# Kernel tuning notes

Hardware: AMD Instinct MI355X
Metric: run time of the kernel (lower is better)

## Reference

```python
import jax, jax.numpy as jnp
import numpy as np
from jax import lax

KH = KW = 3
K = KH * KW
STRIDE = 1
PAD = 1
DIL = 1
GN_GROUPS = 32
EPS = 1e-5


def setup_inputs() -> dict:
    key = jax.random.key(0)
    k0, k1, k2 = jax.random.split(key, 3)
    B, C, H, W = 8, 256, 64, 64
    O = 256
    x = jax.random.normal(k0, (B, C, H, W), jnp.float32)
    # offset-predicting conv (DeformConv2dPack.conv_offset); small weights keep offsets ~O(1)
    w_off = jax.random.normal(k1, (2 * K, C, KH, KW), jnp.float32) * 0.01
    b_off = jnp.zeros((2 * K,), jnp.float32)
    w_dcn = jax.random.normal(k2, (O, C, KH, KW), jnp.float32) * (1.0 / np.sqrt(C * K))
    gamma = jnp.ones((O,), jnp.float32)
    beta = jnp.zeros((O,), jnp.float32)
    return {"x": x, "w_off": w_off, "b_off": b_off, "w_dcn": w_dcn, "gamma": gamma, "beta": beta}


def _deform_conv(x, w_off, b_off, w_dcn):
    B, C, H, W = x.shape
    O = w_dcn.shape[0]
    # offsets via standard conv: [B, 2K, Ho, Wo]; channel layout (k, (dy, dx))
    offset = lax.conv_general_dilated(
        x, w_off, (STRIDE, STRIDE), [(PAD, PAD), (PAD, PAD)],
        rhs_dilation=(DIL, DIL), dimension_numbers=("NCHW", "OIHW", "NCHW"))
    offset = offset + b_off[None, :, None, None]
    Ho, Wo = offset.shape[2], offset.shape[3]
    off = offset.reshape(B, K, 2, Ho, Wo)
    ky = jnp.repeat(jnp.arange(KH), KW)  # [K]
    kx = jnp.tile(jnp.arange(KW), KH)    # [K]
    base_y = (jnp.arange(Ho) * STRIDE - PAD)[None, :, None] + (ky * DIL)[:, None, None]  # [K,Ho,1]
    base_x = (jnp.arange(Wo) * STRIDE - PAD)[None, None, :] + (kx * DIL)[:, None, None]  # [K,1,Wo]
    py = off[:, :, 0] + base_y[None].astype(off.dtype)  # [B,K,Ho,Wo]
    px = off[:, :, 1] + base_x[None].astype(off.dtype)

    def sample_one(xi, py_i, px_i):  # xi [C,H,W]; py/px [K,Ho,Wo]
        y0 = jnp.floor(py_i)
        x0 = jnp.floor(px_i)
        dy = py_i - y0
        dx = px_i - x0
        y0i = y0.astype(jnp.int32)
        x0i = x0.astype(jnp.int32)

        def gather(yi, xj, w):
            valid = (yi >= 0) & (yi < H) & (xj >= 0) & (xj < W)
            yc = jnp.clip(yi, 0, H - 1)
            xc = jnp.clip(xj, 0, W - 1)
            return xi[:, yc, xc] * (w * valid)[None]  # [C,K,Ho,Wo]

        return (gather(y0i, x0i, (1 - dy) * (1 - dx))
                + gather(y0i, x0i + 1, (1 - dy) * dx)
                + gather(y0i + 1, x0i, dy * (1 - dx))
                + gather(y0i + 1, x0i + 1, dy * dx))

    cols = jax.vmap(sample_one)(x, py, px)  # [B,C,K,Ho,Wo]
    y = jnp.einsum("ock,bckp->bop", w_dcn.reshape(O, C, K),
                   cols.reshape(B, C, K, Ho * Wo))
    return y.reshape(B, O, Ho, Wo)


def _group_norm(y, gamma, beta):
    B, O, Ho, Wo = y.shape
    g = y.reshape(B, GN_GROUPS, O // GN_GROUPS, Ho, Wo)
    mean = g.mean(axis=(2, 3, 4), keepdims=True)
    var = g.var(axis=(2, 3, 4), keepdims=True)
    yn = ((g - mean) * lax.rsqrt(var + EPS)).reshape(B, O, Ho, Wo)
    return yn * gamma[None, :, None, None] + beta[None, :, None, None]


def reference(x, w_off, b_off, w_dcn, gamma, beta):
    y = _deform_conv(x, w_off, b_off, w_dcn)
    y = _group_norm(y, gamma, beta)
    return y * jnp.tanh(jax.nn.softplus(y))  # Mish
```

## Files before the change

### kernel.cpp

```cpp
#include <hip/hip_runtime.h>
#include <hip/hip_bf16.h>
#include <math.h>

typedef __bf16 bf16x8 __attribute__((ext_vector_type(8)));
typedef float f32x4 __attribute__((ext_vector_type(4)));
typedef float f32x2 __attribute__((ext_vector_type(2)));
typedef unsigned int u32;
typedef u32 u32x4 __attribute__((ext_vector_type(4)));
typedef u32 u32x2 __attribute__((ext_vector_type(2)));


#define FENCE() __builtin_amdgcn_sched_barrier(0)
#define VMCNT(n) do { asm volatile("s_waitcnt vmcnt(" #n ")" ::: "memory"); FENCE(); } while (0)
#define LGKM0() do { asm volatile("s_waitcnt lgkmcnt(0)" ::: "memory"); FENCE(); } while (0)

__device__ inline u32 pack2bf16(float a, float b) {
  u32 ua = __float_as_uint(a);
  u32 ub = __float_as_uint(b);
  ua += 0x7fffu + ((ua >> 16) & 1u);
  ub += 0x7fffu + ((ub >> 16) & 1u);
  return (ua >> 16) | (ub & 0xffff0000u);
}

__global__ void prep(const float* __restrict__ w_dcn, const float* __restrict__ w_off,
                     unsigned short* __restrict__ wT4, unsigned short* __restrict__ wOffT,
                     float* __restrict__ stats) {
  size_t id = (size_t)blockIdx.x * 256 + threadIdx.x;
  if (id < 589824) {
    int o  = (int)(id / 2304);
    int ck = (int)(id % 2304);
    int k = ck >> 8, c = ck & 255;
    float v = w_dcn[(size_t)(o * 256 + c) * 9 + k];
    u32 uv = __float_as_uint(v);
    uv += 0x7fffu + ((uv >> 16) & 1u);
    int tile = ck >> 6, kk = ck & 63;
    int lin = o * 128 + kk * 2;
    int swz = lin ^ ((o & 7) << 4);
    *(unsigned short*)((char*)wT4 + (size_t)tile * 32768 + swz) = (unsigned short)(uv >> 16);
  } else if (id < 663552) {
    int r = (int)(id - 589824);
    int tile = r >> 11;
    int rr = r & 2047;
    int o = rr >> 6, kk = rr & 63;
    int k = tile >> 2, cc = tile & 3;
    int c = (cc << 6) + kk;
    float v = (o < 18) ? w_off[(size_t)(o * 256 + c) * 9 + k] : 0.f;
    u32 uv = __float_as_uint(v);
    uv += 0x7fffu + ((uv >> 16) & 1u);
    int swz = (o * 128 + kk * 2) ^ ((o & 7) << 4);
    *(unsigned short*)((char*)wOffT + (size_t)tile * 4096 + swz) = (unsigned short)(uv >> 16);
  } else if (id < 664064) {
    stats[id - 663552] = 0.f;
  }
}

__global__ __launch_bounds__(256) void transpose_x(const float* __restrict__ x,
                                                   unsigned short* __restrict__ xT) {
  __shared__ float tl[64][65];
  int bx = blockIdx.x;
  int b = bx >> 8;
  int y = (bx >> 2) & 63;
  int cb = (bx & 3) << 6;
  int t = threadIdx.x;
  int xi = t & 63, cr = t >> 6;
  size_t base = (((size_t)(b * 256 + cb) * 64 + y) << 6);
#pragma unroll
  for (int rep = 0; rep < 16; ++rep) {
    int cl = rep * 4 + cr;
    tl[cl][xi] = x[base + (size_t)cl * 4096 + xi];
  }
  __syncthreads();
  int xw = t & 63, cpair = t >> 6;
#pragma unroll
  for (int r = 0; r < 2; ++r) {
    int cgl = cpair * 2 + r;
    int cg = (cb >> 3) + cgl;
    u32 pk4[4];
#pragma unroll
    for (int i = 0; i < 4; ++i)
      pk4[i] = pack2bf16(tl[cgl * 8 + 2 * i][xw], tl[cgl * 8 + 2 * i + 1][xw]);
    u32x4 v = {pk4[0], pk4[1], pk4[2], pk4[3]};
    *(u32x4*)((char*)xT + (((size_t)b << 21)) + ((size_t)cg << 16) + ((y << 6) + xw) * 16) = v;
  }
}

__global__ __launch_bounds__(256) void conv_offset_mfma(
    const unsigned short* __restrict__ xT, const unsigned short* __restrict__ wOffT,
    float* __restrict__ offs) {
  __shared__ union {
    unsigned short Bo[4][2][2048];
    float red[4][64][32];
  } sm;
  const int bx = blockIdx.x;
  const int lb = ((bx & 7) << 6) + (bx >> 3);
  const int b = lb >> 6;
  const int row = lb & 63;
  const int t = threadIdx.x;
  const int lane = t & 63, w = t >> 6;
  const char* xTbB = (const char*)xT + ((size_t)b << 21);

  f32x4 acc[4][2];
#pragma unroll
  for (int i = 0; i < 4; ++i)
#pragma unroll
    for (int j = 0; j < 2; ++j) {
      f32x4 z = {0.f, 0.f, 0.f, 0.f};
      acc[i][j] = z;
    }

  auto stageB = [&](int k, int d) {
    const char* src = (const char*)wOffT + ((size_t)((k << 2) + w) << 12);
    char* dstb = (char*)&sm.Bo[w][d][0];
#pragma unroll
    for (int i2 = 0; i2 < 4; ++i2) {
      __builtin_amdgcn_global_load_lds(
          (const __attribute__((address_space(1))) u32*)(src + (i2 << 10) + (lane << 4)),
          (__attribute__((address_space(3))) u32*)(dstb + (i2 << 10)),
          16, 0, 0);
    }
  };

  stageB(0, 0);
  u32x4 rA[8];
  const u32x4 zv = {0u, 0u, 0u, 0u};

  for (int k = 0; k < 9; ++k) {
    int ky = k / 3, kxv = k - ky * 3;
    int rowp = row - 1 + ky;
    bool rok = ((unsigned)rowp < 64u);
    bool ok[4];
    if (rok) {
      int pix[4];
#pragma unroll
      for (int pg = 0; pg < 4; ++pg) {
        int xs = (pg << 4) + (lane & 15) + kxv - 1;
        ok[pg] = ((unsigned)xs < 64u);
        int xc = min(max(xs, 0), 63);
        pix[pg] = (rowp << 6) + xc;
      }
#pragma unroll
      for (int s = 0; s < 2; ++s) {
        const char* base = xTbB + ((size_t)((w << 3) + (s << 2) + (lane >> 4)) << 16);
#pragma unroll
        for (int pg = 0; pg < 4; ++pg)
          rA[s * 4 + pg] = *(const u32x4*)(base + ((size_t)pix[pg] << 4));
      }
    }
    if (k < 8) stageB(k + 1, (k + 1) & 1);
    VMCNT(4);
    if (rok) {
      const char* Bb = (const char*)&sm.Bo[w][k & 1][0];
#pragma unroll
      for (int s = 0; s < 2; ++s) {
        bf16x8 bb[2];
        int kx = (s << 6) + ((lane >> 4) << 4);
#pragma unroll
        for (int j = 0; j < 2; ++j) {
          int o = (j << 4) + (lane & 15);
          bb[j] = *(const bf16x8*)(Bb + o * 128 + (kx ^ ((o & 7) << 4)));
        }
#pragma unroll
        for (int pg = 0; pg < 4; ++pg) {
          u32x4 av = ok[pg] ? rA[s * 4 + pg] : zv;
          bf16x8 af = __builtin_bit_cast(bf16x8, av);
#pragma unroll
          for (int j = 0; j < 2; ++j)
            acc[pg][j] = __builtin_amdgcn_mfma_f32_16x16x32_bf16(af, bb[j], acc[pg][j], 0, 0, 0);
        }
      }
    }
  }

#pragma unroll
  for (int pg = 0; pg < 4; ++pg)
#pragma unroll
    for (int j = 0; j < 2; ++j)
#pragma unroll
      for (int r = 0; r < 4; ++r) {
        int px = (pg << 4) + ((lane >> 4) << 2) + r;
        int o = (j << 4) + (lane & 15);
        sm.red[w][px][o] = acc[pg][j][r];
      }
  __syncthreads();
  {
    int px = t >> 2, oq = (t & 3) << 3;
#pragma unroll
    for (int e = 0; e < 8; ++e) {
      int o = oq + e;
      if (o < 18) {
        float sv = sm.red[0][px][o] + sm.red[1][px][o]
                 + sm.red[2][px][o] + sm.red[3][px][o];
        offs[((size_t)b * 4096 + (row << 6) + px) * 18 + o] = sv;
      }
    }
  }
}

union ArenaM {
  struct {
    unsigned short A[2][128][64];
    unsigned short Bt[3][16384];
  } m;
  unsigned short ytile[256][136];
};

__global__ __launch_bounds__(512) void dcn_main(
    const unsigned short* __restrict__ xT, const float* __restrict__ offs,
    const float* __restrict__ boff, const unsigned short* __restrict__ wT4,
    unsigned short* __restrict__ yb, float* __restrict__ stats) {
  __shared__ ArenaM ar;
  __shared__ u32 pcor[9][128][2];
  __shared__ float pwt[9][128][4];

  const int bx = blockIdx.x;
  const int lb = ((bx & 7) << 5) + (bx >> 3);
  const int b = lb >> 5;
  const int pxbase = (lb & 31) << 7;
  const int t = threadIdx.x;
  const int lane = t & 63, wid = t >> 6;
  const char* xTbB = (const char*)xT + ((size_t)b << 21);
  const int pxs = ((wid & 1) << 6) + lane;
  const int gp = (wid >> 1) << 1;
  const int wr = wid >> 2, wc = wid & 3;
  const int obase = wc << 6;

  for (int idx = t; idx < 1152; idx += 512) {
    int k = idx >> 7, px = idx & 127;
    int pxg = pxbase + px;
    int yy = pxg >> 6, xx = pxg & 63;
    int ky = k / 3, kx = k - ky * 3;
    const float* op = offs + ((size_t)b * 4096 + pxg) * 18 + k * 2;
    float py = op[0] + boff[k * 2] + (float)(yy - 1 + ky);
    float pxf = op[1] + boff[k * 2 + 1] + (float)(xx - 1 + kx);
    float fy = floorf(py), fx = floorf(pxf);
    float dy = py - fy, dx = pxf - fx;
    int y0 = (int)fy, x0 = (int)fx;
    int y1 = y0 + 1, x1 = x0 + 1;
    float vy0 = ((unsigned)y0 < 64u) ? 1.f : 0.f;
    float vy1 = ((unsigned)y1 < 64u) ? 1.f : 0.f;
    float vx0 = ((unsigned)x0 < 64u) ? 1.f : 0.f;
    float vx1 = ((unsigned)x1 < 64u) ? 1.f : 0.f;
    int y0c = min(max(y0, 0), 63), y1c = min(max(y1, 0), 63);
    int x0c = min(max(x0, 0), 63), x1c = min(max(x1, 0), 63);
    pcor[k][px][0] = (u32)((y0c << 6) + x0c) | ((u32)((y0c << 6) + x1c) << 16);
    pcor[k][px][1] = (u32)((y1c << 6) + x0c) | ((u32)((y1c << 6) + x1c) << 16);
    pwt[k][px][0] = (1.f - dy) * (1.f - dx) * vy0 * vx0;
    pwt[k][px][1] = (1.f - dy) * dx * vy0 * vx1;
    pwt[k][px][2] = dy * (1.f - dx) * vy1 * vx0;
    pwt[k][px][3] = dy * dx * vy1 * vx1;
  }

  f32x4 acc[4][4];
#pragma unroll
  for (int i = 0; i < 4; ++i)
#pragma unroll
    for (int j = 0; j < 4; ++j) {
      f32x4 z = {0.f, 0.f, 0.f, 0.f};
      acc[i][j] = z;
    }

  __syncthreads();

  u32x4 rA[8];

  auto issueA = [&](int tt) {
    int k = tt >> 2, cc = tt & 3;
    u32 c01 = pcor[k][pxs][0], c23 = pcor[k][pxs][1];
    const char* p0 = xTbB + ((size_t)((cc << 3) + gp) << 16);
#pragma unroll
    for (int g = 0; g < 2; ++g) {
      const char* bgp = p0 + ((size_t)g << 16);
      rA[g * 4 + 0] = *(const u32x4*)(bgp + ((size_t)(c01 & 0xffffu) << 4));
      rA[g * 4 + 1] = *(const u32x4*)(bgp + ((size_t)(c01 >> 16) << 4));
      rA[g * 4 + 2] = *(const u32x4*)(bgp + ((size_t)(c23 & 0xffffu) << 4));
      rA[g * 4 + 3] = *(const u32x4*)(bgp + ((size_t)(c23 >> 16) << 4));
    }
  };
  auto issueB = [&](int tt, int bufi) {
    const char* src = (const char*)wT4 + ((size_t)tt << 15) + (wid << 12);
    char* dstb = (char*)&ar.m.Bt[bufi][0] + (wid << 12);
#pragma unroll
    for (int i2 = 0; i2 < 4; ++i2) {
      __builtin_amdgcn_global_load_lds(
          (const __attribute__((address_space(1))) u32*)(src + (i2 << 10) + (lane << 4)),
          (__attribute__((address_space(3))) u32*)(dstb + (i2 << 10)),
          16, 0, 0);
    }
  };
  auto blendA = [&](int tt) {
    int k = tt >> 2;
    f32x4 w = *(const f32x4*)&pwt[k][pxs][0];
    char* dst = (char*)&ar.m.A[tt & 1][0][0] + pxs * 128;
    int sw = (pxs & 7) << 4;
#pragma unroll
    for (int g = 0; g < 2; ++g) {
      u32 o4[4];
#pragma unroll
      for (int e = 0; e < 4; ++e) {
        u32 u0 = rA[g * 4 + 0][e], u1 = rA[g * 4 + 1][e];
        u32 u2 = rA[g * 4 + 2][e], u3 = rA[g * 4 + 3][e];
        float lo = w[0] * __uint_as_float(u0 << 16);
        lo = fmaf(w[1], __uint_as_float(u1 << 16), lo);
        lo = fmaf(w[2], __uint_as_float(u2 << 16), lo);
        lo = fmaf(w[3], __uint_as_float(u3 << 16), lo);
        float hi = w[0] * __uint_as_float(u0 & 0xffff0000u);
        hi = fmaf(w[1], __uint_as_float(u1 & 0xffff0000u), hi);
        hi = fmaf(w[2], __uint_as_float(u2 & 0xffff0000u), hi);
        hi = fmaf(w[3], __uint_as_float(u3 & 0xffff0000u), hi);
        asm("v_cvt_pk_bf16_f32 %0, %1, %2" : "=v"(o4[e]) : "v"(lo), "v"(hi));
      }
      u32x4 ov = {o4[0], o4[1], o4[2], o4[3]};
      *(u32x4*)(dst + (((gp + g) << 4) ^ sw)) = ov;
    }
  };

  issueA(0); FENCE();
  issueB(0, 0); FENCE();
  VMCNT(4);
  blendA(0);
  FENCE();
  issueA(1); FENCE();
  issueB(1, 1); FENCE();
  VMCNT(12);
  LGKM0();
  __builtin_amdgcn_s_barrier();

  int bm3 = 0;
  for (int tt = 0; tt < 36; ++tt) {
    {
      const char* Ab = (const char*)&ar.m.A[tt & 1][0][0];
      const char* Bb = (const char*)&ar.m.Bt[bm3][0];
      __builtin_amdgcn_s_setprio(1);
#pragma unroll
      for (int s = 0; s < 2; ++s) {
        int kx = (s << 6) + ((lane >> 4) << 4);
        bf16x8 a[4], bb[4];
#pragma unroll
        for (int i = 0; i < 4; ++i) {
          int r16 = (wr << 6) + (i << 4) + (lane & 15);
          a[i] = *(const bf16x8*)(Ab + r16 * 128 + (kx ^ ((r16 & 7) << 4)));
        }
#pragma unroll
        for (int j = 0; j < 4; ++j) {
          int o = obase + (j << 4) + (lane & 15);
          bb[j] = *(const bf16x8*)(Bb + o * 128 + (kx ^ ((o & 7) << 4)));
        }
#pragma unroll
        for (int i = 0; i < 4; ++i)
#pragma unroll
          for (int j = 0; j < 4; ++j)
            acc[i][j] = __builtin_amdgcn_mfma_f32_16x16x32_bf16(a[i], bb[j], acc[i][j], 0, 0, 0);
      }
      __builtin_amdgcn_s_setprio(0);
    }
    FENCE();
    if (tt < 35) {
      VMCNT(4);
      blendA(tt + 1);
      FENCE();
      if (tt < 34) {
        issueA(tt + 2); FENCE();
        int bn = bm3 + 2; if (bn >= 3) bn -= 3;
        issueB(tt + 2, bn); FENCE();
      }
    }
    if (tt == 34) { VMCNT(0); }
    else { VMCNT(12); }
    LGKM0();
    __builtin_amdgcn_s_barrier();
    FENCE();
    bm3 = (bm3 == 2) ? 0 : bm3 + 1;
  }

#pragma unroll
  for (int j = 0; j < 4; ++j) {
    float s1 = 0.f, s2 = 0.f;
#pragma unroll
    for (int i = 0; i < 4; ++i)
#pragma unroll
      for (int r = 0; r < 4; ++r) {
        float v = acc[i][j][r];
        s1 += v;
        s2 += v * v;
      }
    s1 += __shfl_xor(s1, 1, 64);  s2 += __shfl_xor(s2, 1, 64);
    s1 += __shfl_xor(s1, 2, 64);  s2 += __shfl_xor(s2, 2, 64);
    s1 += __shfl_xor(s1, 4, 64);  s2 += __shfl_xor(s2, 4, 64);
    s1 += __shfl_xor(s1, 16, 64); s2 += __shfl_xor(s2, 16, 64);
    s1 += __shfl_xor(s1, 32, 64); s2 += __shfl_xor(s2, 32, 64);
    if ((lane & 0x37) == 0) {
      int g = (obase + (j << 4) + (lane & 15)) >> 3;
      atomicAdd(&stats[((b << 5) + g) * 2 + 0], s1);
      atomicAdd(&stats[((b << 5) + g) * 2 + 1], s2);
    }
  }

#pragma unroll
  for (int i = 0; i < 4; ++i)
#pragma unroll
    for (int j = 0; j < 4; ++j) {
      int o = obase + (j << 4) + (lane & 15);
      int pxr = (wr << 6) + (i << 4) + ((lane >> 4) << 2);
      u32 wv0, wv1;
      asm("v_cvt_pk_bf16_f32 %0, %1, %2" : "=v"(wv0) : "v"(acc[i][j][0]), "v"(acc[i][j][1]));
      asm("v_cvt_pk_bf16_f32 %0, %1, %2" : "=v"(wv1) : "v"(acc[i][j][2]), "v"(acc[i][j][3]));
      u32x2 wv = {wv0, wv1};
      *(u32x2*)((char*)ar.ytile + o * 272 + pxr * 2) = wv;
    }
  __syncthreads();
  {
    int o = t >> 1, half = t & 1;
    const char* srcb = (const char*)ar.ytile + o * 272 + (half << 7);
    unsigned short* dst = yb + (((size_t)(b * 256 + o)) << 12) + pxbase + (half << 6);
#pragma unroll
    for (int qq = 0; qq < 8; ++qq)
      *(u32x4*)((char*)dst + (qq << 4)) = *(const u32x4*)(srcb + (qq << 4));
  }
}

__global__ __launch_bounds__(256) void gn_mish(const unsigned short* __restrict__ yb,
                                               const float* __restrict__ stats,
                                               const float* __restrict__ gamma,
                                               const float* __restrict__ beta,
                                               float* __restrict__ out) {
  int v = blockIdx.x * 512 + threadIdx.x;
#pragma unroll
  for (int it = 0; it < 2; ++it, v += 256) {
    int o = (v >> 9) & 255;
    int b = v >> 17;
    float s1 = stats[((b << 5) + (o >> 3)) * 2 + 0];
    float s2 = stats[((b << 5) + (o >> 3)) * 2 + 1];
    float mean = s1 * (1.f / 32768.f);
    float var = s2 * (1.f / 32768.f) - mean * mean;
    float rstd = rsqrtf(var + 1e-5f);
    float ga = gamma[o] * rstd, be = beta[o] - mean * gamma[o] * rstd;
    u32x4 u = *(const u32x4*)(yb + ((size_t)v << 3));
    float res[8];
#pragma unroll
    for (int e = 0; e < 4; ++e) {
      float va = __uint_as_float(u[e] << 16);
      float vb = __uint_as_float(u[e] & 0xffff0000u);
      float v0 = fmaf(va, ga, be);
      float v1 = fmaf(vb, ga, be);
      float e0 = expf(fminf(v0, 15.f));
      float e1 = expf(fminf(v1, 15.f));
      float n0 = e0 * (e0 + 2.f);
      float n1 = e1 * (e1 + 2.f);
      float m0 = v0 * (n0 / (n0 + 2.f));
      float m1 = v1 * (n1 / (n1 + 2.f));
      if (v0 > 15.f) m0 = v0;
      if (v1 > 15.f) m1 = v1;
      res[2 * e] = m0;
      res[2 * e + 1] = m1;
    }
    f32x4 o0 = {res[0], res[1], res[2], res[3]};
    f32x4 o1 = {res[4], res[5], res[6], res[7]};
    float* dst = out + ((size_t)v << 3);
    *(f32x4*)dst = o0;
    *((f32x4*)dst + 1) = o1;
  }
}

extern "C" void kernel_launch(void* const* d_in, const int* in_sizes, int n_in,
                              void* d_out, int out_size, void* d_ws, size_t ws_size,
                              hipStream_t stream) {
  const float* x     = (const float*)d_in[0];
  const float* w_off = (const float*)d_in[1];
  const float* b_off = (const float*)d_in[2];
  const float* w_dcn = (const float*)d_in[3];
  const float* gamma = (const float*)d_in[4];
  const float* beta  = (const float*)d_in[5];
  float* out = (float*)d_out;
  char* ws = (char*)d_ws;
  unsigned short* xT   = (unsigned short*)(ws);
  unsigned short* yb   = (unsigned short*)(ws + 16777216);
  float* offs          = (float*)(ws + 33554432);
  unsigned short* wT4  = (unsigned short*)(ws + 35913728);
  unsigned short* wOffT= (unsigned short*)(ws + 37093376);
  float* stats         = (float*)(ws + 37240832);
  prep<<<dim3(2594), dim3(256), 0, stream>>>(w_dcn, w_off, wT4, wOffT, stats);
  transpose_x<<<dim3(2048), dim3(256), 0, stream>>>(x, xT);
  conv_offset_mfma<<<dim3(512), dim3(256), 0, stream>>>(xT, wOffT, offs);
  dcn_main<<<dim3(256), dim3(512), 0, stream>>>(xT, offs, b_off, wT4, yb, stats);
  gn_mish<<<dim3(2048), dim3(256), 0, stream>>>(yb, stats, gamma, beta, out);
}
```

Before: 115.2 us.

## Shrink dcn_main tile to one 64-pixel row per 256-thread block

```diff
diff --git a/kernel.cpp b/kernel.cpp
--- a/kernel.cpp
+++ b/kernel.cpp
@@ -198,40 +198,49 @@
 
 union ArenaM {
   struct {
-    unsigned short A[2][128][64];
-    unsigned short Bt[3][16384];
+    unsigned short A[2][64][64];
+    unsigned short Bt[2][16384];
   } m;
-  unsigned short ytile[256][136];
+  unsigned short ytile[256][72];
 };
 
-__global__ __launch_bounds__(512) void dcn_main(
+__global__ __launch_bounds__(256) void dcn_main(
     const unsigned short* __restrict__ xT, const float* __restrict__ offs,
     const float* __restrict__ boff, const unsigned short* __restrict__ wT4,
     unsigned short* __restrict__ yb, float* __restrict__ stats) {
   __shared__ ArenaM ar;
-  __shared__ u32 pcor[9][128][2];
-  __shared__ float pwt[9][128][4];
+  __shared__ float sboff[18];
 
   const int bx = blockIdx.x;
-  const int lb = ((bx & 7) << 5) + (bx >> 3);
-  const int b = lb >> 5;
-  const int pxbase = (lb & 31) << 7;
+  const int lb = ((bx & 7) << 6) + (bx >> 3);
+  const int b = lb >> 6;
+  const int row = lb & 63;
+  const int pxbase = row << 6;
   const int t = threadIdx.x;
   const int lane = t & 63, wid = t >> 6;
   const char* xTbB = (const char*)xT + ((size_t)b << 21);
-  const int pxs = ((wid & 1) << 6) + lane;
-  const int gp = (wid >> 1) << 1;
-  const int wr = wid >> 2, wc = wid & 3;
-  const int obase = wc << 6;
-
-  for (int idx = t; idx < 1152; idx += 512) {
-    int k = idx >> 7, px = idx & 127;
-    int pxg = pxbase + px;
-    int yy = pxg >> 6, xx = pxg & 63;
+  const int gp = wid << 1;
+  const int obase = wid << 6;
+
+  if (t < 18) sboff[t] = boff[t];
+
+  f32x4 acc[4][4];
+#pragma unroll
+  for (int i = 0; i < 4; ++i)
+#pragma unroll
+    for (int j = 0; j < 4; ++j) {
+      f32x4 z = {0.f, 0.f, 0.f, 0.f};
+      acc[i][j] = z;
+    }
+
+  __syncthreads();
+
+  auto cparams = [&](int k, u32& c01, u32& c23, f32x4& w4) {
     int ky = k / 3, kx = k - ky * 3;
-    const float* op = offs + ((size_t)b * 4096 + pxg) * 18 + k * 2;
-    float py = op[0] + boff[k * 2] + (float)(yy - 1 + ky);
-    float pxf = op[1] + boff[k * 2 + 1] + (float)(xx - 1 + kx);
+    const float* op = offs + ((size_t)b * 4096 + pxbase + lane) * 18 + k * 2;
+    f32x2 o2 = *(const f32x2*)op;
+    float py = o2[0] + sboff[k * 2] + (float)(row - 1 + ky);
+    float pxf = o2[1] + sboff[k * 2 + 1] + (float)(lane - 1 + kx);
     float fy = floorf(py), fx = floorf(pxf);
     float dy = py - fy, dx = pxf - fx;
     int y0 = (int)fy, x0 = (int)fx;
@@ -242,31 +251,18 @@
     float vx1 = ((unsigned)x1 < 64u) ? 1.f : 0.f;
     int y0c = min(max(y0, 0), 63), y1c = min(max(y1, 0), 63);
     int x0c = min(max(x0, 0), 63), x1c = min(max(x1, 0), 63);
-    pcor[k][px][0] = (u32)((y0c << 6) + x0c) | ((u32)((y0c << 6) + x1c) << 16);
-    pcor[k][px][1] = (u32)((y1c << 6) + x0c) | ((u32)((y1c << 6) + x1c) << 16);
-    pwt[k][px][0] = (1.f - dy) * (1.f - dx) * vy0 * vx0;
-    pwt[k][px][1] = (1.f - dy) * dx * vy0 * vx1;
-    pwt[k][px][2] = dy * (1.f - dx) * vy1 * vx0;
-    pwt[k][px][3] = dy * dx * vy1 * vx1;
-  }
-
-  f32x4 acc[4][4];
-#pragma unroll
-  for (int i = 0; i < 4; ++i)
-#pragma unroll
-    for (int j = 0; j < 4; ++j) {
-      f32x4 z = {0.f, 0.f, 0.f, 0.f};
-      acc[i][j] = z;
-    }
-
-  __syncthreads();
+    c01 = (u32)((y0c << 6) + x0c) | ((u32)((y0c << 6) + x1c) << 16);
+    c23 = (u32)((y1c << 6) + x0c) | ((u32)((y1c << 6) + x1c) << 16);
+    w4[0] = (1.f - dy) * (1.f - dx) * vy0 * vx0;
+    w4[1] = (1.f - dy) * dx * vy0 * vx1;
+    w4[2] = dy * (1.f - dx) * vy1 * vx0;
+    w4[3] = dy * dx * vy1 * vx1;
+  };
 
   u32x4 rA[8];
 
-  auto issueA = [&](int tt) {
-    int k = tt >> 2, cc = tt & 3;
-    u32 c01 = pcor[k][pxs][0], c23 = pcor[k][pxs][1];
-    const char* p0 = xTbB + ((size_t)((cc << 3) + gp) << 16);
+  auto issueA = [&](int ccq, u32 c01, u32 c23) {
+    const char* p0 = xTbB + ((size_t)((ccq << 3) + gp) << 16);
 #pragma unroll
     for (int g = 0; g < 2; ++g) {
       const char* bgp = p0 + ((size_t)g << 16);
@@ -276,22 +272,20 @@
       rA[g * 4 + 3] = *(const u32x4*)(bgp + ((size_t)(c23 >> 16) << 4));
     }
   };
-  auto issueB = [&](int tt, int bufi) {
-    const char* src = (const char*)wT4 + ((size_t)tt << 15) + (wid << 12);
-    char* dstb = (char*)&ar.m.Bt[bufi][0] + (wid << 12);
-#pragma unroll
-    for (int i2 = 0; i2 < 4; ++i2) {
+  auto issueB = [&](int tt, int d) {
+    const char* src = (const char*)wT4 + ((size_t)tt << 15) + (wid << 13);
+    char* dstb = (char*)&ar.m.Bt[d][0] + (wid << 13);
+#pragma unroll
+    for (int i2 = 0; i2 < 8; ++i2) {
       __builtin_amdgcn_global_load_lds(
           (const __attribute__((address_space(1))) u32*)(src + (i2 << 10) + (lane << 4)),
           (__attribute__((address_space(3))) u32*)(dstb + (i2 << 10)),
           16, 0, 0);
     }
   };
-  auto blendA = [&](int tt) {
-    int k = tt >> 2;
-    f32x4 w = *(const f32x4*)&pwt[k][pxs][0];
-    char* dst = (char*)&ar.m.A[tt & 1][0][0] + pxs * 128;
-    int sw = (pxs & 7) << 4;
+  auto blendA = [&](int d, f32x4 w) {
+    char* dst = (char*)&ar.m.A[d][0][0] + lane * 128;
+    int sw = (lane & 7) << 4;
 #pragma unroll
     for (int g = 0; g < 2; ++g) {
       u32 o4[4];
@@ -314,62 +308,69 @@
     }
   };
 
-  issueA(0); FENCE();
+  u32 cur01, cur23, nxt01 = 0, nxt23 = 0;
+  f32x4 curw, nxtw = {0.f, 0.f, 0.f, 0.f};
+  cparams(0, cur01, cur23, curw);
+  issueA(0, cur01, cur23); FENCE();
   issueB(0, 0); FENCE();
-  VMCNT(4);
-  blendA(0);
+  VMCNT(8);
+  blendA(0, curw);
   FENCE();
-  issueA(1); FENCE();
-  issueB(1, 1); FENCE();
-  VMCNT(12);
+  issueA(1, cur01, cur23); FENCE();
+  VMCNT(8);
   LGKM0();
   __builtin_amdgcn_s_barrier();
-
-  int bm3 = 0;
-  for (int tt = 0; tt < 36; ++tt) {
-    {
-      const char* Ab = (const char*)&ar.m.A[tt & 1][0][0];
-      const char* Bb = (const char*)&ar.m.Bt[bm3][0];
-      __builtin_amdgcn_s_setprio(1);
-#pragma unroll
-      for (int s = 0; s < 2; ++s) {
-        int kx = (s << 6) + ((lane >> 4) << 4);
-        bf16x8 a[4], bb[4];
-#pragma unroll
-        for (int i = 0; i < 4; ++i) {
-          int r16 = (wr << 6) + (i << 4) + (lane & 15);
-          a[i] = *(const bf16x8*)(Ab + r16 * 128 + (kx ^ ((r16 & 7) << 4)));
+  FENCE();
+
+  for (int k = 0; k < 9; ++k) {
+    if (k < 8) cparams(k + 1, nxt01, nxt23, nxtw);
+#pragma unroll
+    for (int cc = 0; cc < 4; ++cc) {
+      const int tt = (k << 2) + cc;
+      const int d = cc & 1;
+      if (tt < 35) {
+        issueB(tt + 1, d ^ 1); FENCE();
+        VMCNT(8);
+      }
+      {
+        const char* Ab = (const char*)&ar.m.A[d][0][0];
+        const char* Bb = (const char*)&ar.m.Bt[d][0];
+        __builtin_amdgcn_s_setprio(1);
+#pragma unroll
+        for (int s = 0; s < 2; ++s) {
+          int kx = (s << 6) + ((lane >> 4) << 4);
+          bf16x8 a[4], bb[4];
+#pragma unroll
+          for (int i = 0; i < 4; ++i) {
+            int r16 = (i << 4) + (lane & 15);
+            a[i] = *(const bf16x8*)(Ab + r16 * 128 + (kx ^ ((r16 & 7) << 4)));
+          }
+#pragma unroll
+          for (int j = 0; j < 4; ++j) {
+            int o = obase + (j << 4) + (lane & 15);
+            bb[j] = *(const bf16x8*)(Bb + o * 128 + (kx ^ ((o & 7) << 4)));
+          }
+#pragma unroll
+          for (int i = 0; i < 4; ++i)
+#pragma unroll
+            for (int j = 0; j < 4; ++j)
+              acc[i][j] = __builtin_amdgcn_mfma_f32_16x16x32_bf16(a[i], bb[j], acc[i][j], 0, 0, 0);
         }
-#pragma unroll
-        for (int j = 0; j < 4; ++j) {
-          int o = obase + (j << 4) + (lane & 15);
-          bb[j] = *(const bf16x8*)(Bb + o * 128 + (kx ^ ((o & 7) << 4)));
-        }
-#pragma unroll
-        for (int i = 0; i < 4; ++i)
-#pragma unroll
-          for (int j = 0; j < 4; ++j)
-            acc[i][j] = __builtin_amdgcn_mfma_f32_16x16x32_bf16(a[i], bb[j], acc[i][j], 0, 0, 0);
-      }
-      __builtin_amdgcn_s_setprio(0);
-    }
-    FENCE();
-    if (tt < 35) {
-      VMCNT(4);
-      blendA(tt + 1);
+        if (tt < 35) blendA(d ^ 1, (cc == 3) ? nxtw : curw);
+        __builtin_amdgcn_s_setprio(0);
+      }
       FENCE();
       if (tt < 34) {
-        issueA(tt + 2); FENCE();
-        int bn = bm3 + 2; if (bn >= 3) bn -= 3;
-        issueB(tt + 2, bn); FENCE();
-      }
-    }
-    if (tt == 34) { VMCNT(0); }
-    else { VMCNT(12); }
-    LGKM0();
-    __builtin_amdgcn_s_barrier();
-    FENCE();
-    bm3 = (bm3 == 2) ? 0 : bm3 + 1;
+        issueA((cc + 2) & 3, (cc >= 2) ? nxt01 : cur01, (cc >= 2) ? nxt23 : cur23);
+        FENCE();
+      }
+      if (tt == 34) { VMCNT(0); }
+      else if (tt < 34) { VMCNT(8); }
+      LGKM0();
+      __builtin_amdgcn_s_barrier();
+      FENCE();
+    }
+    cur01 = nxt01; cur23 = nxt23; curw = nxtw;
   }
 
 #pragma unroll
@@ -400,18 +401,18 @@
 #pragma unroll
     for (int j = 0; j < 4; ++j) {
       int o = obase + (j << 4) + (lane & 15);
-      int pxr = (wr << 6) + (i << 4) + ((lane >> 4) << 2);
+      int pxr = (i << 4) + ((lane >> 4) << 2);
       u32 wv0, wv1;
       asm("v_cvt_pk_bf16_f32 %0, %1, %2" : "=v"(wv0) : "v"(acc[i][j][0]), "v"(acc[i][j][1]));
       asm("v_cvt_pk_bf16_f32 %0, %1, %2" : "=v"(wv1) : "v"(acc[i][j][2]), "v"(acc[i][j][3]));
       u32x2 wv = {wv0, wv1};
-      *(u32x2*)((char*)ar.ytile + o * 272 + pxr * 2) = wv;
+      *(u32x2*)((char*)ar.ytile + o * 144 + pxr * 2) = wv;
     }
   __syncthreads();
   {
-    int o = t >> 1, half = t & 1;
-    const char* srcb = (const char*)ar.ytile + o * 272 + (half << 7);
-    unsigned short* dst = yb + (((size_t)(b * 256 + o)) << 12) + pxbase + (half << 6);
+    int o = t;
+    const char* srcb = (const char*)ar.ytile + o * 144;
+    unsigned short* dst = yb + (((size_t)(b * 256 + o)) << 12) + pxbase;
 #pragma unroll
     for (int qq = 0; qq < 8; ++qq)
       *(u32x4*)((char*)dst + (qq << 4)) = *(const u32x4*)(srcb + (qq << 4));
@@ -481,6 +482,6 @@
   prep<<<dim3(2594), dim3(256), 0, stream>>>(w_dcn, w_off, wT4, wOffT, stats);
   transpose_x<<<dim3(2048), dim3(256), 0, stream>>>(x, xT);
   conv_offset_mfma<<<dim3(512), dim3(256), 0, stream>>>(xT, wOffT, offs);
-  dcn_main<<<dim3(256), dim3(512), 0, stream>>>(xT, offs, b_off, wT4, yb, stats);
+  dcn_main<<<dim3(512), dim3(256), 0, stream>>>(xT, offs, b_off, wT4, yb, stats);
   gn_mish<<<dim3(2048), dim3(256), 0, stream>>>(yb, stats, gamma, beta, out);
 }
```

Result: slower. 158.6 us (+37.6%).
